# Optimization experiments

Hardware: AMD Instinct MI355X
Metric: run time of the kernel (lower is better)

The kernel has to match this reference:

```python
import jax, jax.numpy as jnp
import numpy as np

N_NODES = 50000
N_EDGES = 800000
IN_C, HID_C, OUT_C = 256, 256, 64


def _glorot(key, shape):
    fan_in, fan_out = shape[1], shape[0]
    lim = float(np.sqrt(6.0 / (fan_in + fan_out)))
    return jax.random.uniform(key, shape, jnp.float32, -lim, lim)


def setup_inputs() -> dict:
    key = jax.random.key(0)
    ks = jax.random.split(key, 8)
    x = jax.random.normal(ks[0], (N_NODES, IN_C), jnp.float32)
    edge_index = jax.random.randint(ks[1], (2, N_EDGES), 0, N_NODES, jnp.int64)
    # layer 1: SAGEConv(IN_C -> HID_C): lin_l (agg neighbors, has bias), lin_r (root, no bias)
    W_l1 = _glorot(ks[2], (HID_C, IN_C))
    b1 = jnp.zeros((HID_C,), jnp.float32)
    W_r1 = _glorot(ks[3], (HID_C, IN_C))
    # layer 2: SAGEConv(HID_C -> OUT_C)
    W_l2 = _glorot(ks[4], (OUT_C, HID_C))
    b2 = jnp.zeros((OUT_C,), jnp.float32)
    W_r2 = _glorot(ks[5], (OUT_C, HID_C))
    return {"x": x, "W_l1": W_l1, "b1": b1, "W_r1": W_r1,
            "W_l2": W_l2, "b2": b2, "W_r2": W_r2, "edge_index": edge_index}


def _sage_conv(x, src, dst, W_l, b, W_r, n_nodes):
    # mean aggregation of source-node features into destination nodes
    msg = x[src]                                               # [E, C]
    agg = jax.ops.segment_sum(msg, dst, num_segments=n_nodes)  # [N, C]
    deg = jax.ops.segment_sum(jnp.ones((src.shape[0],), x.dtype), dst,
                              num_segments=n_nodes)            # [N]
    agg = agg / jnp.maximum(deg, 1.0)[:, None]
    # out = lin_l(agg) + lin_r(x); bias only on lin_l (PyG SAGEConv default)
    return agg @ W_l.T + b + x @ W_r.T


def reference(x, W_l1, b1, W_r1, W_l2, b2, W_r2, edge_index):
    src, dst = edge_index[0], edge_index[1]
    n = x.shape[0]
    h = _sage_conv(x, src, dst, W_l1, b1, W_r1, n)
    h = jax.nn.relu(h)  # dropout is identity in eval mode
    out = _sage_conv(h, src, dst, W_l2, b2, W_r2, n)
    return out
```

## Files before the change

kernel.cpp:

```cpp
#include <hip/hip_runtime.h>

#define IN_C 256
#define HID_C 256
#define OUT_C 64

#define NBK 64
#define NPAD 50176
#define N2 (NPAD / 2)
#define NCH (NPAD / 256)

typedef __attribute__((ext_vector_type(8))) short bf16x8;
typedef __attribute__((ext_vector_type(4))) float f32x4;
typedef __attribute__((ext_vector_type(2))) float f32x2;
typedef __attribute__((ext_vector_type(8))) unsigned short ushortx8;
typedef __attribute__((ext_vector_type(4))) unsigned int u32x4;
typedef __attribute__((ext_vector_type(2))) unsigned int u32x2;

__device__ inline float b2f(unsigned short u) {
    union { unsigned int u; float f; } v; v.u = ((unsigned int)u) << 16; return v.f;
}
__device__ inline unsigned short f2b(float f) {
    union { float f; unsigned int u; } v; v.f = f;
    unsigned int u = v.u;
    unsigned int r = (u + 0x7fffu + ((u >> 16) & 1u)) >> 16;
    return (unsigned short)r;
}

__device__ __forceinline__ unsigned char f2fp8(float v) {
    int pk = __builtin_amdgcn_cvt_pk_fp8_f32(v, v, 0, false);
    return (unsigned char)(pk & 0xff);
}
__device__ __forceinline__ void fp8acc4(unsigned int w, float& a0, float& a1, float& a2, float& a3) {
    f32x2 lo = __builtin_amdgcn_cvt_pk_f32_fp8((int)w, false);
    f32x2 hi = __builtin_amdgcn_cvt_pk_f32_fp8((int)w, true);
    a0 += lo.x; a1 += lo.y; a2 += hi.x; a3 += hi.y;
}

__device__ __forceinline__ void gl2lds16(const ushort* g, ushort* l) {
    __builtin_amdgcn_global_load_lds((const __attribute__((address_space(1))) void*)g,
                                     (__attribute__((address_space(3))) void*)l, 16, 0, 0);
}

__device__ __forceinline__ void conv8(const float* __restrict__ src, ushort* __restrict__ dst, int u) {
    const float4* p = (const float4*)(src + (size_t)u * 8);
    float4 a = p[0], b = p[1];
    ushort4 o0 = make_ushort4(f2b(a.x), f2b(a.y), f2b(a.z), f2b(a.w));
    ushort4 o1 = make_ushort4(f2b(b.x), f2b(b.y), f2b(b.z), f2b(b.w));
    ((ushort4*)(dst + (size_t)u * 8))[0] = o0;
    ((ushort4*)(dst + (size_t)u * 8))[1] = o1;
}


__global__ __launch_bounds__(1024) void k_front(const int* __restrict__ dst, int E, int EPB,
                                                ushort* __restrict__ rank,
                                                unsigned int* __restrict__ cnt32,
                                                int* __restrict__ chunkpart,
                                                const float* __restrict__ x, ushort* __restrict__ xb,
                                                int xUnits,
                                                const float* __restrict__ Wl1, const float* __restrict__ Wr1,
                                                const float* __restrict__ Wl2, const float* __restrict__ Wr2,
                                                ushort* __restrict__ Wc1, ushort* __restrict__ Wc2) {
    const int bid = blockIdx.x;
    const int t = threadIdx.x;

    if (bid < NBK) {
        __shared__ unsigned int h[N2];
        for (int i = t; i < N2; i += 1024) h[i] = 0;
        __syncthreads();

        const int e0 = bid * EPB;
        const int e1 = min(e0 + EPB, E);
        for (int e = e0 + t; e < e1; e += 1024) {
            int d = dst[e];
            int sh = (d & 1) << 4;
            unsigned int old = atomicAdd(&h[d >> 1], 1u << sh);
            rank[e] = (ushort)((old >> sh) & 0xffffu);
        }
        __syncthreads();

        unsigned int* outp = cnt32 + (size_t)bid * N2;
        for (int i = t; i < N2; i += 1024) outp[i] = h[i];

        if (t < NCH) {
            int c = t;
            int sum = 0;
#pragma unroll 8
            for (int j = 0; j < 128; ++j) {
                unsigned int v = h[c * 128 + ((j + c) & 127)];
                sum += (int)(v & 0xffffu) + (int)(v >> 16);
            }
            chunkpart[c * NBK + bid] = sum;
        }
        return;
    }

    const int ct = (bid - NBK) * 1024 + t;
    const int cn = 256 * 1024;
    for (int i = ct; i < 20480; i += cn) {
        if (i < 8192)       conv8(Wl1, Wc1,         i);
        else if (i < 16384) conv8(Wr1, Wc1 + 65536, i - 8192);
        else if (i < 18432) conv8(Wl2, Wc2,         i - 16384);
        else                conv8(Wr2, Wc2 + 16384, i - 18432);
    }
    for (int u = ct; u < xUnits; u += cn) conv8(x, xb, u);
}


__global__ __launch_bounds__(256) void k_scan(const unsigned int* __restrict__ cnt32,
                                              const int* __restrict__ chunkpart, int N,
                                              int* __restrict__ row_start,
                                              ushort* __restrict__ off16) {
    __shared__ int s[256];
    const int bid = blockIdx.x;
    const int t = threadIdx.x;

    int pre = 0;
    const int limit = bid * NBK;
    for (int i = t; i < limit; i += 256) pre += chunkpart[i];
    s[t] = pre;
    __syncthreads();
    for (int o = 128; o > 0; o >>= 1) {
        if (t < o) s[t] += s[t + o];
        __syncthreads();
    }
    const int chunk_off = s[0];
    __syncthreads();

    const int i = bid * 256 + t;
    const ushort* cnt16 = (const ushort*)cnt32;
    int run = 0;
#pragma unroll 8
    for (int b = 0; b < NBK; ++b) {
        ushort cv = cnt16[(size_t)b * NPAD + i];
        off16[(size_t)b * NPAD + i] = (ushort)run;
        run += cv;
    }
    int deg = run;

    s[t] = deg;
    __syncthreads();
    for (int o = 1; o < 256; o <<= 1) {
        int xx = (t >= o) ? s[t - o] : 0;
        __syncthreads();
        s[t] += xx;
        __syncthreads();
    }
    if (i < N) row_start[i + 1] = s[t] + chunk_off;
    if (i == 0) row_start[0] = 0;
}


__global__ __launch_bounds__(256) void k_scatter(const int* __restrict__ src,
                                                 const int* __restrict__ dst,
                                                 const ushort* __restrict__ rank,
                                                 const int* __restrict__ row_start,
                                                 const ushort* __restrict__ off16,
                                                 int E, int EPB, int per,
                                                 int* __restrict__ eidx) {
    const int e0 = blockIdx.x * per;
    const int e1 = min(e0 + per, E);
    for (int e = e0 + (int)threadIdx.x; e < e1; e += 256) {
        int d = dst[e];
        int b = e / EPB;
        eidx[row_start[d] + (int)off16[(size_t)b * NPAD + d] + (int)rank[e]] = src[e];
    }
}


__global__ __launch_bounds__(256) void k_gemm_l1(const ushort* __restrict__ A,
                                                 const ushort* __restrict__ W,
                                                 unsigned char* __restrict__ Cp,
                                                 ushort* __restrict__ Cr,
                                                 int N) {
    __shared__ ushort Aall[64 * 256];
    __shared__ ushort Wb[2 * 128 * 64];

    const int bx = blockIdx.x;
    const int t = threadIdx.x;
    const int bm = bx * 64;

    const int wid  = t >> 6;
    const int lane = t & 63;
    const int wr = wid >> 1;
    const int wc = wid & 1;
    const int lr = lane & 15;
    const int lk = lane >> 4;

    {
        const int arow7 = (t >> 5) & 7;
        const int asrc  = ((t & 31) ^ arow7) << 3;
#pragma unroll
        for (int i = 0; i < 8; ++i) {
            gl2lds16(A + (size_t)(bm + i * 8 + (t >> 5)) * 256 + asrc,
                     Aall + i * 2048 + t * 8);
        }
        const int wrow7 = (t >> 3) & 7;
        const int wsrc  = ((t & 7) ^ wrow7) << 3;
#pragma unroll
        for (int i = 0; i < 4; ++i) {
            gl2lds16(W + (size_t)(i * 32 + (t >> 3)) * 256 + 0 + wsrc,
                     Wb + i * 2048 + t * 8);
        }
    }
    __syncthreads();

    f32x4 acc[2][4];
    int s = 0;
#pragma unroll
    for (int by = 0; by < 4; ++by) {
#pragma unroll
        for (int m = 0; m < 2; ++m)
#pragma unroll
            for (int n = 0; n < 4; ++n) acc[m][n] = (f32x4){0.f, 0.f, 0.f, 0.f};

#pragma unroll
        for (int kk = 0; kk < 4; ++kk, ++s) {
            const int sn = s + 1;
            if (sn < 16) {
                const int by_n = sn >> 2, kk_n = sn & 3, buf_n = sn & 1;
                const int wrow7 = (t >> 3) & 7;
                const int wsrc  = ((t & 7) ^ wrow7) << 3;
#pragma unroll
                for (int i = 0; i < 4; ++i) {
                    gl2lds16(W + (size_t)(by_n * 128 + i * 32 + (t >> 3)) * 256 + kk_n * 64 + wsrc,
                             Wb + buf_n * 8192 + i * 2048 + t * 8);
                }
            }

            const int kb = kk * 8;
            const int buf = s & 1;
            const int sw = lr & 7;
#pragma unroll
            for (int ks = 0; ks < 2; ++ks) {
                bf16x8 a[2], b[4];
                const int ck = ks * 4 + lk;
#pragma unroll
                for (int m = 0; m < 2; ++m)
                    a[m] = *(const bf16x8*)(Aall + (wr * 32 + m * 16 + lr) * 256 + ((kb + (ck ^ sw)) << 3));
#pragma unroll
                for (int n = 0; n < 4; ++n)
                    b[n] = *(const bf16x8*)(Wb + buf * 8192 + (wc * 64 + n * 16 + lr) * 64 + ((ck ^ sw) << 3));
#pragma unroll
                for (int m = 0; m < 2; ++m)
#pragma unroll
                    for (int n = 0; n < 4; ++n)
                        acc[m][n] = __builtin_amdgcn_mfma_f32_16x16x32_bf16(a[m], b[n], acc[m][n], 0, 0, 0);
            }

            if (kk == 3) {
                const bool isP = (by * 128 + wc * 64) < HID_C;
#pragma unroll
                for (int m = 0; m < 2; ++m)
#pragma unroll
                    for (int r2 = 0; r2 < 4; ++r2) {
                        int row = bm + wr * 32 + m * 16 + lk * 4 + r2;
                        if (row < N) {
                            if (isP) {
#pragma unroll
                                for (int n = 0; n < 4; ++n) {
                                    int col = by * 128 + wc * 64 + n * 16 + lr;
                                    Cp[(size_t)row * HID_C + col] = f2fp8(acc[m][n][r2]);
                                }
                            } else {
#pragma unroll
                                for (int n = 0; n < 4; ++n) {
                                    int col = by * 128 + wc * 64 + n * 16 + lr - HID_C;
                                    Cr[(size_t)row * HID_C + col] = f2b(acc[m][n][r2]);
                                }
                            }
                        }
                    }
            }
            __syncthreads();
        }
    }
}


__global__ __launch_bounds__(256) void k_gemm_mfma(const ushort* __restrict__ A,
                                                   const ushort* __restrict__ W,
                                                   unsigned char* __restrict__ Cp,
                                                   ushort* __restrict__ Cr,
                                                   int N, int K, int PC, int nby, int nwg) {
    __shared__ ushort As[2][128 * 64];
    __shared__ ushort Bs[2][128 * 64];

    const int orig = blockIdx.x;
    const int q = nwg >> 3, r = nwg & 7;
    const int xcd = orig & 7;
    const int base = (xcd < r) ? xcd * (q + 1) : r * (q + 1) + (xcd - r) * q;
    const int wgid = base + (orig >> 3);
    const int bx = wgid / nby, by = wgid % nby;

    const int wid  = threadIdx.x >> 6;
    const int lane = threadIdx.x & 63;
    const int wr = wid >> 1, wc = wid & 1;
    const int bm = bx * 128;
    const int bn = by * 128;
    const int lr = lane & 15;
    const int lk = lane >> 4;
    const int srow   = lane >> 3;
    const int schunk = lane & 7;

    f32x4 acc[4][4];
#pragma unroll
    for (int m = 0; m < 4; ++m)
#pragma unroll
        for (int n = 0; n < 4; ++n) acc[m][n] = (f32x4){0.f, 0.f, 0.f, 0.f};

#pragma unroll
    for (int i = 0; i < 4; ++i) {
        int seg = wid * 4 + i;
        int row = seg * 8 + srow;
        gl2lds16(A + (size_t)(bm + row) * K + schunk * 8, As[0] + seg * 512);
        gl2lds16(W + (size_t)(bn + row) * K + schunk * 8, Bs[0] + seg * 512);
    }
    __syncthreads();

    int cur = 0;
    for (int k0 = 0; k0 < K; k0 += 64) {
        const int kn = k0 + 64;
        if (kn < K) {
#pragma unroll
            for (int i = 0; i < 4; ++i) {
                int seg = wid * 4 + i;
                int row = seg * 8 + srow;
                gl2lds16(A + (size_t)(bm + row) * K + kn + schunk * 8, As[cur ^ 1] + seg * 512);
                gl2lds16(W + (size_t)(bn + row) * K + kn + schunk * 8, Bs[cur ^ 1] + seg * 512);
            }
        }

#pragma unroll
        for (int ks = 0; ks < 2; ++ks) {
            bf16x8 a[4], b[4];
#pragma unroll
            for (int m = 0; m < 4; ++m)
                a[m] = *(const bf16x8*)(As[cur] + (wr * 64 + m * 16 + lr) * 64 + ks * 32 + lk * 8);
#pragma unroll
            for (int n = 0; n < 4; ++n)
                b[n] = *(const bf16x8*)(Bs[cur] + (wc * 64 + n * 16 + lr) * 64 + ks * 32 + lk * 8);
#pragma unroll
            for (int m = 0; m < 4; ++m)
#pragma unroll
                for (int n = 0; n < 4; ++n)
                    acc[m][n] = __builtin_amdgcn_mfma_f32_16x16x32_bf16(a[m], b[n], acc[m][n], 0, 0, 0);
        }
        __syncthreads();
        cur ^= 1;
    }

    const bool isP = (bn + wc * 64) < PC;
#pragma unroll
    for (int m = 0; m < 4; ++m)
#pragma unroll
        for (int r2 = 0; r2 < 4; ++r2) {
            int row = bm + wr * 64 + m * 16 + lk * 4 + r2;
            if (row < N) {
                if (isP) {
#pragma unroll
                    for (int n = 0; n < 4; ++n) {
                        int col = bn + wc * 64 + n * 16 + lr;
                        Cp[(size_t)row * PC + col] = f2fp8(acc[m][n][r2]);
                    }
                } else {
#pragma unroll
                    for (int n = 0; n < 4; ++n) {
                        int col = bn + wc * 64 + n * 16 + lr - PC;
                        Cr[(size_t)row * PC + col] = f2b(acc[m][n][r2]);
                    }
                }
            }
        }
}


__global__ __launch_bounds__(256) void k_agg1(const unsigned char* __restrict__ P1,
                                              const ushort* __restrict__ R1,
                                              const float* __restrict__ bias,
                                              const int* __restrict__ row_start,
                                              const int* __restrict__ eidx,
                                              ushort* __restrict__ h, int N) {
    int node = (blockIdx.x * blockDim.x + threadIdx.x) >> 6;
    int lane = threadIdx.x & 63;
    if (node >= N) return;
    const int slot = lane >> 4;
    const int sub  = lane & 15;
    int s0 = row_start[node], s1 = row_start[node + 1];

    float acc[16];
#pragma unroll
    for (int i = 0; i < 16; ++i) acc[i] = 0.f;

    for (int e = s0 + slot; e < s1; e += 16) {
        int e1 = e + 4, e2 = e + 8, e3 = e + 12;
        bool h1 = e1 < s1, h2 = e2 < s1, h3 = e3 < s1;
        int sA = eidx[e];
        int sB = h1 ? eidx[e1] : sA;
        int sC = h2 ? eidx[e2] : sA;
        int sD = h3 ? eidx[e3] : sA;
        u32x4 a = *(const u32x4*)(P1 + (size_t)sA * 256 + sub * 16);
        u32x4 b = *(const u32x4*)(P1 + (size_t)sB * 256 + sub * 16);
        u32x4 c = *(const u32x4*)(P1 + (size_t)sC * 256 + sub * 16);
        u32x4 d = *(const u32x4*)(P1 + (size_t)sD * 256 + sub * 16);
#pragma unroll
        for (int w = 0; w < 4; ++w) fp8acc4(a[w], acc[w*4], acc[w*4+1], acc[w*4+2], acc[w*4+3]);
        if (h1) {
#pragma unroll
            for (int w = 0; w < 4; ++w) fp8acc4(b[w], acc[w*4], acc[w*4+1], acc[w*4+2], acc[w*4+3]);
        }
        if (h2) {
#pragma unroll
            for (int w = 0; w < 4; ++w) fp8acc4(c[w], acc[w*4], acc[w*4+1], acc[w*4+2], acc[w*4+3]);
        }
        if (h3) {
#pragma unroll
            for (int w = 0; w < 4; ++w) fp8acc4(d[w], acc[w*4], acc[w*4+1], acc[w*4+2], acc[w*4+3]);
        }
    }

#pragma unroll
    for (int i = 0; i < 16; ++i) {
        acc[i] += __shfl_xor(acc[i], 16, 64);
        acc[i] += __shfl_xor(acc[i], 32, 64);
    }

    if (slot == 0) {
        int d = s1 - s0;
        float inv = 1.0f / (float)(d > 1 ? d : 1);
        const ushort* rp = R1 + (size_t)node * 256 + sub * 16;
        ushortx8 r0 = *(const ushortx8*)(rp);
        ushortx8 r1 = *(const ushortx8*)(rp + 8);
        const float* bp = bias + sub * 16;
        ushortx8 o0, o1;
#pragma unroll
        for (int i = 0; i < 8; ++i) {
            float v0 = fmaxf(acc[i] * inv + bp[i] + b2f(r0[i]), 0.f);
            float v1 = fmaxf(acc[i + 8] * inv + bp[i + 8] + b2f(r1[i]), 0.f);
            o0[i] = f2b(v0);
            o1[i] = f2b(v1);
        }
        ushort* hp = h + (size_t)node * 256 + sub * 16;
        *(ushortx8*)(hp) = o0;
        *(ushortx8*)(hp + 8) = o1;
    }
}


__global__ __launch_bounds__(256) void k_agg2(const unsigned char* __restrict__ P2,
                                              const ushort* __restrict__ R2,
                                              const float* __restrict__ bias,
                                              const int* __restrict__ row_start,
                                              const int* __restrict__ eidx,
                                              float* __restrict__ out, int N) {
    int node = (blockIdx.x * blockDim.x + threadIdx.x) >> 6;
    int lane = threadIdx.x & 63;
    if (node >= N) return;
    const int slot = lane >> 3;
    const int sub  = lane & 7;
    int s0 = row_start[node], s1 = row_start[node + 1];

    float acc[8];
#pragma unroll
    for (int i = 0; i < 8; ++i) acc[i] = 0.f;

    for (int e = s0 + slot; e < s1; e += 32) {
        int e1 = e + 8, e2 = e + 16, e3 = e + 24;
        bool h1 = e1 < s1, h2 = e2 < s1, h3 = e3 < s1;
        int sA = eidx[e];
        int sB = h1 ? eidx[e1] : sA;
        int sC = h2 ? eidx[e2] : sA;
        int sD = h3 ? eidx[e3] : sA;
        u32x2 a = *(const u32x2*)(P2 + (size_t)sA * 64 + sub * 8);
        u32x2 b = *(const u32x2*)(P2 + (size_t)sB * 64 + sub * 8);
        u32x2 c = *(const u32x2*)(P2 + (size_t)sC * 64 + sub * 8);
        u32x2 d = *(const u32x2*)(P2 + (size_t)sD * 64 + sub * 8);
#pragma unroll
        for (int w = 0; w < 2; ++w) fp8acc4(a[w], acc[w*4], acc[w*4+1], acc[w*4+2], acc[w*4+3]);
        if (h1) {
#pragma unroll
            for (int w = 0; w < 2; ++w) fp8acc4(b[w], acc[w*4], acc[w*4+1], acc[w*4+2], acc[w*4+3]);
        }
        if (h2) {
#pragma unroll
            for (int w = 0; w < 2; ++w) fp8acc4(c[w], acc[w*4], acc[w*4+1], acc[w*4+2], acc[w*4+3]);
        }
        if (h3) {
#pragma unroll
            for (int w = 0; w < 2; ++w) fp8acc4(d[w], acc[w*4], acc[w*4+1], acc[w*4+2], acc[w*4+3]);
        }
    }

#pragma unroll
    for (int i = 0; i < 8; ++i) {
        acc[i] += __shfl_xor(acc[i], 8, 64);
        acc[i] += __shfl_xor(acc[i], 16, 64);
        acc[i] += __shfl_xor(acc[i], 32, 64);
    }

    if (slot == 0) {
        int d = s1 - s0;
        float inv = 1.0f / (float)(d > 1 ? d : 1);
        ushortx8 rv = *(const ushortx8*)(R2 + (size_t)node * 64 + sub * 8);
        const float* bp = bias + sub * 8;
        float o[8];
#pragma unroll
        for (int i = 0; i < 8; ++i) o[i] = acc[i] * inv + bp[i] + b2f(rv[i]);
        float4* op = (float4*)(out + (size_t)node * 64 + sub * 8);
        op[0] = make_float4(o[0], o[1], o[2], o[3]);
        op[1] = make_float4(o[4], o[5], o[6], o[7]);
    }
}


extern "C" void kernel_launch(void* const* d_in, const int* in_sizes, int n_in,
                              void* d_out, int out_size, void* d_ws, size_t ws_size,
                              hipStream_t stream) {
    const float* x    = (const float*)d_in[0];
    const float* W_l1 = (const float*)d_in[1];
    const float* b1   = (const float*)d_in[2];
    const float* W_r1 = (const float*)d_in[3];
    const float* W_l2 = (const float*)d_in[4];
    const float* b2   = (const float*)d_in[5];
    const float* W_r2 = (const float*)d_in[6];
    const int*   ei   = (const int*)d_in[7];

    const int N = in_sizes[0] / IN_C;
    const int E = in_sizes[7] / 2;
    const int EPB = (E + NBK - 1) / NBK;
    const int* src = ei;
    const int* dst = ei + E;

    char* ws = (char*)d_ws;
    size_t off_ = 0;
    auto alloc = [&](size_t bytes) -> void* {
        void* p = ws + off_;
        off_ += (bytes + 255) & ~(size_t)255;
        return p;
    };
    unsigned int*  cnt32     = (unsigned int*)alloc((size_t)NBK * N2 * 4);
    ushort*        off16     = (ushort*)alloc((size_t)NBK * NPAD * 2);
    int*           chunkpart = (int*)alloc((size_t)NCH * NBK * 4);
    int*           row_start = (int*)alloc((size_t)(N + 1) * 4);
    ushort*        rank      = (ushort*)alloc((size_t)E * 2);
    int*           eidx      = (int*)alloc((size_t)E * 4);
    ushort*        xb        = (ushort*)alloc((size_t)N * IN_C * 2);
    ushort*        Wc1       = (ushort*)alloc((size_t)2 * HID_C * IN_C * 2);
    ushort*        Wc2       = (ushort*)alloc((size_t)2 * OUT_C * HID_C * 2);
    unsigned char* P1        = (unsigned char*)alloc((size_t)N * HID_C);
    ushort*        R1        = (ushort*)alloc((size_t)N * HID_C * 2);
    ushort*        h         = (ushort*)alloc((size_t)N * HID_C * 2);
    unsigned char* P2        = (unsigned char*)alloc((size_t)N * OUT_C);
    ushort*        R2        = (ushort*)alloc((size_t)N * OUT_C * 2);
    (void)alloc(128 * 512 * 2);
    (void)ws_size; (void)n_in; (void)out_size;

    {
        int xUnits = N * IN_C / 8;
        k_front<<<NBK + 256, 1024, 0, stream>>>(dst, E, EPB, rank, cnt32, chunkpart,
                                                x, xb, xUnits,
                                                W_l1, W_r1, W_l2, W_r2, Wc1, Wc2);
    }

    k_scan<<<NCH, 256, 0, stream>>>(cnt32, chunkpart, N, row_start, off16);

    {
        const int nScat = 448;
        const int per = (E + nScat - 1) / nScat;
        k_scatter<<<nScat, 256, 0, stream>>>(src, dst, rank, row_start, off16,
                                             E, EPB, per, eidx);
    }

    {
        int nbx = (N + 63) / 64;
        k_gemm_l1<<<nbx, 256, 0, stream>>>(xb, Wc1, P1, R1, N);
        k_agg1<<<(N + 3) / 4, 256, 0, stream>>>(P1, R1, b1, row_start, eidx, h, N);
    }

    {
        int nbx = (N + 127) / 128, nby = (2 * OUT_C) / 128;
        int nwg = nbx * nby;
        k_gemm_mfma<<<nwg, 256, 0, stream>>>(h, Wc2, P2, R2, N, HID_C, OUT_C, nby, nwg);
        k_agg2<<<(N + 3) / 4, 256, 0, stream>>>(P2, R2, b2, row_start, eidx, (float*)d_out, N);
    }
}
```

Before: 160.0 us.

## Fuse edge scatter into layer-1 GEMM launch and keep weights resident in LDS

The edge scatter kernel is merged into the layer-1 GEMM launch as extra blocks, so CSR construction and the projection GEMM run concurrently and one launch disappears. Both GEMMs are restructured to load a full 128x256 weight slice into LDS once per block, with an XCD-aware block remap. The A operand is now read directly from global memory into registers instead of being staged in LDS. This removes the per-k-step syncs and double buffering. It relies on L2 and cache hits for the A reads, and the 64KB LDS footprint may limit occupancy.

```diff
diff --git a/kernel.cpp b/kernel.cpp
--- a/kernel.cpp
+++ b/kernel.cpp
@@ -150,227 +150,201 @@
 }
 
 
-__global__ __launch_bounds__(256) void k_scatter(const int* __restrict__ src,
-                                                 const int* __restrict__ dst,
-                                                 const ushort* __restrict__ rank,
-                                                 const int* __restrict__ row_start,
-                                                 const ushort* __restrict__ off16,
-                                                 int E, int EPB, int per,
-                                                 int* __restrict__ eidx) {
-    const int e0 = blockIdx.x * per;
-    const int e1 = min(e0 + per, E);
-    for (int e = e0 + (int)threadIdx.x; e < e1; e += 256) {
-        int d = dst[e];
-        int b = e / EPB;
-        eidx[row_start[d] + (int)off16[(size_t)b * NPAD + d] + (int)rank[e]] = src[e];
-    }
-}
-
-
 __global__ __launch_bounds__(256) void k_gemm_l1(const ushort* __restrict__ A,
                                                  const ushort* __restrict__ W,
                                                  unsigned char* __restrict__ Cp,
                                                  ushort* __restrict__ Cr,
-                                                 int N) {
-    __shared__ ushort Aall[64 * 256];
-    __shared__ ushort Wb[2 * 128 * 64];
-
-    const int bx = blockIdx.x;
+                                                 int N, int nScat, int nwg,
+                                                 const int* __restrict__ src, const int* __restrict__ dst,
+                                                 const ushort* __restrict__ rank,
+                                                 const int* __restrict__ row_start,
+                                                 const ushort* __restrict__ off16,
+                                                 int E, int EPB, int per, int* __restrict__ eidx) {
+    if (blockIdx.x < (unsigned)nScat) {
+        const int e0 = blockIdx.x * per;
+        const int e1 = min(e0 + per, E);
+        for (int e = e0 + (int)threadIdx.x; e < e1; e += 256) {
+            int d = dst[e];
+            int b = e / EPB;
+            eidx[row_start[d] + (int)off16[(size_t)b * NPAD + d] + (int)rank[e]] = src[e];
+        }
+        return;
+    }
+
+    __shared__ ushort Wt[128 * 256];
+
+    const int orig = blockIdx.x - nScat;
+    const int q = nwg >> 3, r = nwg & 7;
+    const int xcd = orig & 7;
+    const int base = (xcd < r) ? xcd * (q + 1) : r * (q + 1) + (xcd - r) * q;
+    const int wgid = base + (orig >> 3);
+    const int bx = wgid >> 2, by = wgid & 3;
+
     const int t = threadIdx.x;
-    const int bm = bx * 64;
+
+    {
+        const int col8 = t >> 5;
+        const int srcc = (t & 31) ^ (col8 & 7);
+#pragma unroll
+        for (int p = 0; p < 16; ++p) {
+            gl2lds16(W + (size_t)(by * 128 + p * 8 + col8) * 256 + srcc * 8,
+                     Wt + p * 2048 + t * 8);
+        }
+    }
+    __syncthreads();
 
     const int wid  = t >> 6;
     const int lane = t & 63;
-    const int wr = wid >> 1;
-    const int wc = wid & 1;
+    const int wr = wid >> 1, wc = wid & 1;
     const int lr = lane & 15;
     const int lk = lane >> 4;
-
-    {
-        const int arow7 = (t >> 5) & 7;
-        const int asrc  = ((t & 31) ^ arow7) << 3;
-#pragma unroll
-        for (int i = 0; i < 8; ++i) {
-            gl2lds16(A + (size_t)(bm + i * 8 + (t >> 5)) * 256 + asrc,
-                     Aall + i * 2048 + t * 8);
-        }
-        const int wrow7 = (t >> 3) & 7;
-        const int wsrc  = ((t & 7) ^ wrow7) << 3;
-#pragma unroll
-        for (int i = 0; i < 4; ++i) {
-            gl2lds16(W + (size_t)(i * 32 + (t >> 3)) * 256 + 0 + wsrc,
-                     Wb + i * 2048 + t * 8);
-        }
-    }
-    __syncthreads();
-
-    f32x4 acc[2][4];
-    int s = 0;
-#pragma unroll
-    for (int by = 0; by < 4; ++by) {
+    const int bm = bx * 256;
+    const bool isP = (by * 128 + wc * 64) < HID_C;
+
+#pragma unroll
+    for (int rt = 0; rt < 4; ++rt) {
+        f32x4 acc[2][4];
 #pragma unroll
         for (int m = 0; m < 2; ++m)
 #pragma unroll
             for (int n = 0; n < 4; ++n) acc[m][n] = (f32x4){0.f, 0.f, 0.f, 0.f};
 
-#pragma unroll
-        for (int kk = 0; kk < 4; ++kk, ++s) {
-            const int sn = s + 1;
-            if (sn < 16) {
-                const int by_n = sn >> 2, kk_n = sn & 3, buf_n = sn & 1;
-                const int wrow7 = (t >> 3) & 7;
-                const int wsrc  = ((t & 7) ^ wrow7) << 3;
-#pragma unroll
-                for (int i = 0; i < 4; ++i) {
-                    gl2lds16(W + (size_t)(by_n * 128 + i * 32 + (t >> 3)) * 256 + kk_n * 64 + wsrc,
-                             Wb + buf_n * 8192 + i * 2048 + t * 8);
-                }
-            }
-
-            const int kb = kk * 8;
-            const int buf = s & 1;
-            const int sw = lr & 7;
+        const int rowb = bm + rt * 64 + wr * 32;
+#pragma unroll
+        for (int kk = 0; kk < 4; ++kk) {
 #pragma unroll
             for (int ks = 0; ks < 2; ++ks) {
                 bf16x8 a[2], b[4];
-                const int ck = ks * 4 + lk;
 #pragma unroll
                 for (int m = 0; m < 2; ++m)
-                    a[m] = *(const bf16x8*)(Aall + (wr * 32 + m * 16 + lr) * 256 + ((kb + (ck ^ sw)) << 3));
-#pragma unroll
-                for (int n = 0; n < 4; ++n)
-                    b[n] = *(const bf16x8*)(Wb + buf * 8192 + (wc * 64 + n * 16 + lr) * 64 + ((ck ^ sw) << 3));
+                    a[m] = *(const bf16x8*)(A + (size_t)(rowb + m * 16 + lr) * 256
+                                              + kk * 64 + ks * 32 + lk * 8);
+#pragma unroll
+                for (int n = 0; n < 4; ++n) {
+                    const int col  = wc * 64 + n * 16 + lr;
+                    const int slot = kk * 8 + ((ks * 4 + lk) ^ (lr & 7));
+                    b[n] = *(const bf16x8*)(Wt + col * 256 + slot * 8);
+                }
 #pragma unroll
                 for (int m = 0; m < 2; ++m)
 #pragma unroll
                     for (int n = 0; n < 4; ++n)
                         acc[m][n] = __builtin_amdgcn_mfma_f32_16x16x32_bf16(a[m], b[n], acc[m][n], 0, 0, 0);
             }
-
-            if (kk == 3) {
-                const bool isP = (by * 128 + wc * 64) < HID_C;
-#pragma unroll
-                for (int m = 0; m < 2; ++m)
-#pragma unroll
-                    for (int r2 = 0; r2 < 4; ++r2) {
-                        int row = bm + wr * 32 + m * 16 + lk * 4 + r2;
-                        if (row < N) {
-                            if (isP) {
-#pragma unroll
-                                for (int n = 0; n < 4; ++n) {
-                                    int col = by * 128 + wc * 64 + n * 16 + lr;
-                                    Cp[(size_t)row * HID_C + col] = f2fp8(acc[m][n][r2]);
-                                }
-                            } else {
-#pragma unroll
-                                for (int n = 0; n < 4; ++n) {
-                                    int col = by * 128 + wc * 64 + n * 16 + lr - HID_C;
-                                    Cr[(size_t)row * HID_C + col] = f2b(acc[m][n][r2]);
-                                }
-                            }
+        }
+
+#pragma unroll
+        for (int m = 0; m < 2; ++m)
+#pragma unroll
+            for (int r2 = 0; r2 < 4; ++r2) {
+                int row = rowb + m * 16 + lk * 4 + r2;
+                if (row < N) {
+                    if (isP) {
+#pragma unroll
+                        for (int n = 0; n < 4; ++n) {
+                            int col = by * 128 + wc * 64 + n * 16 + lr;
+                            Cp[(size_t)row * HID_C + col] = f2fp8(acc[m][n][r2]);
+                        }
+                    } else {
+#pragma unroll
+                        for (int n = 0; n < 4; ++n) {
+                            int col = by * 128 + wc * 64 + n * 16 + lr - HID_C;
+                            Cr[(size_t)row * HID_C + col] = f2b(acc[m][n][r2]);
                         }
                     }
+                }
             }
-            __syncthreads();
-        }
-    }
-}
-
-
-__global__ __launch_bounds__(256) void k_gemm_mfma(const ushort* __restrict__ A,
-                                                   const ushort* __restrict__ W,
-                                                   unsigned char* __restrict__ Cp,
-                                                   ushort* __restrict__ Cr,
-                                                   int N, int K, int PC, int nby, int nwg) {
-    __shared__ ushort As[2][128 * 64];
-    __shared__ ushort Bs[2][128 * 64];
+    }
+}
+
+
+__global__ __launch_bounds__(256) void k_gemm_l2(const ushort* __restrict__ A,
+                                                 const ushort* __restrict__ W,
+                                                 unsigned char* __restrict__ Cp,
+                                                 ushort* __restrict__ Cr,
+                                                 int N, int nwg) {
+    __shared__ ushort Wt[128 * 256];
 
     const int orig = blockIdx.x;
     const int q = nwg >> 3, r = nwg & 7;
     const int xcd = orig & 7;
     const int base = (xcd < r) ? xcd * (q + 1) : r * (q + 1) + (xcd - r) * q;
-    const int wgid = base + (orig >> 3);
-    const int bx = wgid / nby, by = wgid % nby;
-
-    const int wid  = threadIdx.x >> 6;
-    const int lane = threadIdx.x & 63;
+    const int bx = base + (orig >> 3);
+
+    const int t = threadIdx.x;
+    {
+        const int col8 = t >> 5;
+        const int srcc = (t & 31) ^ (col8 & 7);
+#pragma unroll
+        for (int p = 0; p < 16; ++p) {
+            gl2lds16(W + (size_t)(p * 8 + col8) * 256 + srcc * 8,
+                     Wt + p * 2048 + t * 8);
+        }
+    }
+    __syncthreads();
+
+    const int wid  = t >> 6;
+    const int lane = t & 63;
     const int wr = wid >> 1, wc = wid & 1;
-    const int bm = bx * 128;
-    const int bn = by * 128;
     const int lr = lane & 15;
     const int lk = lane >> 4;
-    const int srow   = lane >> 3;
-    const int schunk = lane & 7;
-
-    f32x4 acc[4][4];
-#pragma unroll
-    for (int m = 0; m < 4; ++m)
-#pragma unroll
-        for (int n = 0; n < 4; ++n) acc[m][n] = (f32x4){0.f, 0.f, 0.f, 0.f};
-
-#pragma unroll
-    for (int i = 0; i < 4; ++i) {
-        int seg = wid * 4 + i;
-        int row = seg * 8 + srow;
-        gl2lds16(A + (size_t)(bm + row) * K + schunk * 8, As[0] + seg * 512);
-        gl2lds16(W + (size_t)(bn + row) * K + schunk * 8, Bs[0] + seg * 512);
-    }
-    __syncthreads();
-
-    int cur = 0;
-    for (int k0 = 0; k0 < K; k0 += 64) {
-        const int kn = k0 + 64;
-        if (kn < K) {
-#pragma unroll
-            for (int i = 0; i < 4; ++i) {
-                int seg = wid * 4 + i;
-                int row = seg * 8 + srow;
-                gl2lds16(A + (size_t)(bm + row) * K + kn + schunk * 8, As[cur ^ 1] + seg * 512);
-                gl2lds16(W + (size_t)(bn + row) * K + kn + schunk * 8, Bs[cur ^ 1] + seg * 512);
+    const int bm = bx * 128;
+    const bool isP = (wc * 64) < OUT_C;
+
+#pragma unroll
+    for (int rt = 0; rt < 2; ++rt) {
+        f32x4 acc[2][4];
+#pragma unroll
+        for (int m = 0; m < 2; ++m)
+#pragma unroll
+            for (int n = 0; n < 4; ++n) acc[m][n] = (f32x4){0.f, 0.f, 0.f, 0.f};
+
+        const int rowb = bm + rt * 64 + wr * 32;
+#pragma unroll
+        for (int kk = 0; kk < 4; ++kk) {
+#pragma unroll
+            for (int ks = 0; ks < 2; ++ks) {
+                bf16x8 a[2], b[4];
+#pragma unroll
+                for (int m = 0; m < 2; ++m)
+                    a[m] = *(const bf16x8*)(A + (size_t)(rowb + m * 16 + lr) * 256
+                                              + kk * 64 + ks * 32 + lk * 8);
+#pragma unroll
+                for (int n = 0; n < 4; ++n) {
+                    const int col  = wc * 64 + n * 16 + lr;
+                    const int slot = kk * 8 + ((ks * 4 + lk) ^ (lr & 7));
+                    b[n] = *(const bf16x8*)(Wt + col * 256 + slot * 8);
+                }
+#pragma unroll
+                for (int m = 0; m < 2; ++m)
+#pragma unroll
+                    for (int n = 0; n < 4; ++n)
+                        acc[m][n] = __builtin_amdgcn_mfma_f32_16x16x32_bf16(a[m], b[n], acc[m][n], 0, 0, 0);
             }
         }
 
 #pragma unroll
-        for (int ks = 0; ks < 2; ++ks) {
-            bf16x8 a[4], b[4];
-#pragma unroll
-            for (int m = 0; m < 4; ++m)
-                a[m] = *(const bf16x8*)(As[cur] + (wr * 64 + m * 16 + lr) * 64 + ks * 32 + lk * 8);
-#pragma unroll
-            for (int n = 0; n < 4; ++n)
-                b[n] = *(const bf16x8*)(Bs[cur] + (wc * 64 + n * 16 + lr) * 64 + ks * 32 + lk * 8);
-#pragma unroll
-            for (int m = 0; m < 4; ++m)
-#pragma unroll
-                for (int n = 0; n < 4; ++n)
-                    acc[m][n] = __builtin_amdgcn_mfma_f32_16x16x32_bf16(a[m], b[n], acc[m][n], 0, 0, 0);
-        }
-        __syncthreads();
-        cur ^= 1;
-    }
-
-    const bool isP = (bn + wc * 64) < PC;
-#pragma unroll
-    for (int m = 0; m < 4; ++m)
-#pragma unroll
-        for (int r2 = 0; r2 < 4; ++r2) {
-            int row = bm + wr * 64 + m * 16 + lk * 4 + r2;
-            if (row < N) {
-                if (isP) {
-#pragma unroll
-                    for (int n = 0; n < 4; ++n) {
-                        int col = bn + wc * 64 + n * 16 + lr;
-                        Cp[(size_t)row * PC + col] = f2fp8(acc[m][n][r2]);
-                    }
-                } else {
-#pragma unroll
-                    for (int n = 0; n < 4; ++n) {
-                        int col = bn + wc * 64 + n * 16 + lr - PC;
-                        Cr[(size_t)row * PC + col] = f2b(acc[m][n][r2]);
+        for (int m = 0; m < 2; ++m)
+#pragma unroll
+            for (int r2 = 0; r2 < 4; ++r2) {
+                int row = rowb + m * 16 + lk * 4 + r2;
+                if (row < N) {
+                    if (isP) {
+#pragma unroll
+                        for (int n = 0; n < 4; ++n) {
+                            int col = wc * 64 + n * 16 + lr;
+                            Cp[(size_t)row * OUT_C + col] = f2fp8(acc[m][n][r2]);
+                        }
+                    } else {
+#pragma unroll
+                        for (int n = 0; n < 4; ++n) {
+                            int col = wc * 64 + n * 16 + lr - OUT_C;
+                            Cr[(size_t)row * OUT_C + col] = f2b(acc[m][n][r2]);
+                        }
                     }
                 }
             }
-        }
+    }
 }
 
 
@@ -566,20 +540,17 @@
     {
         const int nScat = 448;
         const int per = (E + nScat - 1) / nScat;
-        k_scatter<<<nScat, 256, 0, stream>>>(src, dst, rank, row_start, off16,
-                                             E, EPB, per, eidx);
+        const int nbx = (N + 255) / 256;
+        const int nwg = nbx * 4;
+        k_gemm_l1<<<nScat + nwg, 256, 0, stream>>>(xb, Wc1, P1, R1, N, nScat, nwg,
+                                                   src, dst, rank, row_start, off16,
+                                                   E, EPB, per, eidx);
+        k_agg1<<<(N + 3) / 4, 256, 0, stream>>>(P1, R1, b1, row_start, eidx, h, N);
     }
 
     {
-        int nbx = (N + 63) / 64;
-        k_gemm_l1<<<nbx, 256, 0, stream>>>(xb, Wc1, P1, R1, N);
-        k_agg1<<<(N + 3) / 4, 256, 0, stream>>>(P1, R1, b1, row_start, eidx, h, N);
-    }
-
-    {
-        int nbx = (N + 127) / 128, nby = (2 * OUT_C) / 128;
-        int nwg = nbx * nby;
-        k_gemm_mfma<<<nwg, 256, 0, stream>>>(h, Wc2, P2, R2, N, HID_C, OUT_C, nby, nwg);
+        const int nwg = (N + 127) / 128;
+        k_gemm_l2<<<nwg, 256, 0, stream>>>(h, Wc2, P2, R2, N, nwg);
         k_agg2<<<(N + 3) / 4, 256, 0, stream>>>(P2, R2, b2, row_start, eidx, (float*)d_out, N);
     }
 }
```

Result: no change. 159.9 us (-0.0%).
